# Performance work log

Measured on AMD Instinct MI355X. Metric: run time of the kernel, lower is better.

Reference implementation:

```python
import jax, jax.numpy as jnp
import numpy as np

N = 100000  # nodes
E = 1600000  # edges
D_IN, D_HID, D_OUT = 128, 128, 64
NEG_SLOPE = 0.2


def gat_conv(x, src, dst, W_src, W_dst, att_src, att_dst, bias, num_nodes):
    # PyG GATConv, heads=1, add_self_loops=False.
    h_src = x @ W_src          # [N, C]
    h_dst = x @ W_dst          # [N, C]
    a_src = (h_src * att_src).sum(-1)   # [N]
    a_dst = (h_dst * att_dst).sum(-1)   # [N]
    logits = jax.nn.leaky_relu(a_src[src] + a_dst[dst], NEG_SLOPE)  # [E]
    # segment softmax over destination neighborhoods
    seg_max = jax.ops.segment_max(logits, dst, num_segments=num_nodes)  # [N]
    e = jnp.exp(logits - seg_max[dst])
    denom = jax.ops.segment_sum(e, dst, num_segments=num_nodes)         # [N]
    alpha = e / (denom[dst] + 1e-16)                                    # [E]
    out = jax.ops.segment_sum(alpha[:, None] * h_src[src], dst, num_segments=num_nodes)  # [N, C]
    return out + bias


def setup_inputs() -> dict:
    key = jax.random.key(0)
    ks = jax.random.split(key, 12)
    x = jax.random.normal(ks[0], (N, D_IN), dtype=jnp.float32)
    edge_index = jax.random.randint(ks[1], (2, E), 0, N, dtype=jnp.int64)
    s1 = 1.0 / np.sqrt(D_IN)
    s2 = 1.0 / np.sqrt(D_HID)
    return {
        "x": x,
        "edge_index": edge_index,
        "W1_src": jax.random.uniform(ks[2], (D_IN, D_HID), jnp.float32, -s1, s1),
        "W1_dst": jax.random.uniform(ks[3], (D_IN, D_HID), jnp.float32, -s1, s1),
        "att1_src": jax.random.uniform(ks[4], (D_HID,), jnp.float32, -s2, s2),
        "att1_dst": jax.random.uniform(ks[5], (D_HID,), jnp.float32, -s2, s2),
        "b1": jnp.zeros((D_HID,), jnp.float32),
        "W2_src": jax.random.uniform(ks[6], (D_HID, D_OUT), jnp.float32, -s2, s2),
        "W2_dst": jax.random.uniform(ks[7], (D_HID, D_OUT), jnp.float32, -s2, s2),
        "att2_src": jax.random.uniform(ks[8], (D_OUT,), jnp.float32, -1.0 / np.sqrt(D_OUT), 1.0 / np.sqrt(D_OUT)),
        "att2_dst": jax.random.uniform(ks[9], (D_OUT,), jnp.float32, -1.0 / np.sqrt(D_OUT), 1.0 / np.sqrt(D_OUT)),
        "b2": jnp.zeros((D_OUT,), jnp.float32),
    }


def reference(x, edge_index, W1_src, W1_dst, att1_src, att1_dst, b1,
              W2_src, W2_dst, att2_src, att2_dst, b2):
    src, dst = edge_index[0], edge_index[1]
    h = gat_conv(x, src, dst, W1_src, W1_dst, att1_src, att1_dst, b1, N)
    h = jax.nn.relu(h)
    out = gat_conv(h, src, dst, W2_src, W2_dst, att2_src, att2_dst, b2, N)
    return out
```

## Files before the change

### kernel.cpp

```cpp
#include <hip/hip_runtime.h>


typedef unsigned long long u64;
typedef float v4f __attribute__((ext_vector_type(4)));
typedef _Float16 v2h __attribute__((ext_vector_type(2)));
typedef __fp16 h8 __attribute__((ext_vector_type(8)));

#define SEL_LO 0x01000504u
#define SEL_HI 0x03020706u

__device__ __forceinline__ void ntstore4(float* p, v4f v) {
    __builtin_nontemporal_store(v, (v4f*)p);
}
__device__ __forceinline__ unsigned h2pack(float a, float b) {
    v2h h;
    h.x = (_Float16)a;
    h.y = (_Float16)b;
    return __builtin_bit_cast(unsigned, h);
}
__device__ __forceinline__ float fdot2u(unsigned u, v2h w, float acc) {
    return __builtin_amdgcn_fdot2(__builtin_bit_cast(v2h, u), w, acc, false);
}
__device__ __forceinline__ v2h pkrtz(float a, float b) {
    return __builtin_bit_cast(v2h, __builtin_amdgcn_cvt_pkrtz(a, b));
}

__device__ void matvec_body(const float* __restrict__ W, const float* __restrict__ a,
                            float* __restrict__ out, int cols, int row) {
    int lane = threadIdx.x & 63;
    float s = 0.f;
    for (int j = lane; j < cols; j += 64) s += W[row * cols + j] * a[j];
#pragma unroll
    for (int o = 32; o; o >>= 1) s += __shfl_xor(s, o, 64);
    if (lane == 0) out[row] = s;
}

template <int C>
__device__ void packw_body(const float* __restrict__ W, uint4* __restrict__ Wp) {
    constexpr int NT = C / 16;
    const int total = 4 * NT * 64;
    for (int e = threadIdx.x; e < total; e += 256) {
        int lane = e & 63;
        int ti = (e >> 6) % NT;
        int t = (e >> 6) / NT;
        int k0 = 32 * t + (lane >> 4) * 8;
        int n = ti * 16 + (lane & 15);
        unsigned u[4];
#pragma unroll
        for (int p = 0; p < 4; ++p)
            u[p] = h2pack(W[(size_t)(k0 + 2 * p) * C + n], W[(size_t)(k0 + 2 * p + 1) * C + n]);
        Wp[e] = make_uint4(u[0], u[1], u[2], u[3]);
    }
}

__global__ __launch_bounds__(256) void setup_kernel(
    const int* __restrict__ dst, int* __restrict__ hist, int E, int nbE,
    const float* __restrict__ W1s, uint4* __restrict__ wp1,
    const float* __restrict__ W2s, uint4* __restrict__ wp2,
    const float* __restrict__ W1d, const float* __restrict__ att1d, float* __restrict__ watt1,
    const float* __restrict__ W2d, const float* __restrict__ att2d, float* __restrict__ watt2) {
    int b = blockIdx.x;
    if (b < nbE) {
        __shared__ int h[256];
        h[threadIdx.x] = 0;
        __syncthreads();
        int base = b * 4096;
        int lim = min(base + 4096, E);
        for (int i = base + threadIdx.x; i < lim; i += 256)
            atomicAdd(&h[__builtin_nontemporal_load(dst + i) >> 9], 1);
        __syncthreads();
        __builtin_nontemporal_store(h[threadIdx.x], hist + b * 256 + threadIdx.x);
    } else if (b == nbE) {
        packw_body<128>(W1s, wp1);
    } else if (b == nbE + 1) {
        packw_body<64>(W2s, wp2);
    } else if (b < nbE + 34) {
        matvec_body(W1d, att1d, watt1, 128, (b - nbE - 2) * 4 + (threadIdx.x >> 6));
    } else {
        matvec_body(W2d, att2d, watt2, 64, (b - nbE - 34) * 4 + (threadIdx.x >> 6));
    }
}

__global__ __launch_bounds__(256) void bscan_kernel(const int* __restrict__ hist, int nbE,
                                                    int* __restrict__ bbase,
                                                    int* __restrict__ gcur,
                                                    int* __restrict__ offs, int N, int E) {
    __shared__ int s[256];
    int t = threadIdx.x;
    int v = 0;
#pragma unroll 4
    for (int b = 0; b < nbE; ++b) v += hist[b * 256 + t];
    s[t] = v;
    __syncthreads();
    for (int o = 1; o < 256; o <<= 1) {
        int u = (t >= o) ? s[t - o] : 0;
        __syncthreads();
        s[t] += u;
        __syncthreads();
    }
    int excl = s[t] - v;
    bbase[t] = excl;
    gcur[t] = excl;
    if (t == 255) { bbase[256] = E; offs[N] = E; }
}

__device__ void scatter_body(const int* __restrict__ src, const int* __restrict__ dst,
                             int* __restrict__ gcur, u64* __restrict__ pairs, int E,
                             int blk, char* smem) {
    int* h = (int*)smem;
    int* sbase = h + 256;
    int* rbase = h + 512;
    u64* buf = (u64*)(smem + 3072);
    const int tid = threadIdx.x;
    h[tid] = 0;
    __syncthreads();
    const int base = blk * 4096;
    const int lim = min(4096, E - base);
    u64 pv[16];
    int rk[16];
    int bk[16];
#pragma unroll 16
    for (int k = 0; k < 16; ++k) {
        int i = base + k * 256 + tid;
        if (i < E) {
            int d = __builtin_nontemporal_load(dst + i);
            int b = d >> 9;
            bk[k] = b;
            pv[k] = ((u64)(unsigned)d << 32) | (unsigned)__builtin_nontemporal_load(src + i);
            rk[k] = atomicAdd(&h[b], 1);
        } else {
            bk[k] = -1;
        }
    }
    __syncthreads();
    const int v = h[tid];
    sbase[tid] = v;
    __syncthreads();
    for (int o = 1; o < 256; o <<= 1) {
        int uu = (tid >= o) ? sbase[tid - o] : 0;
        __syncthreads();
        sbase[tid] += uu;
        __syncthreads();
    }
    const int excl = sbase[tid] - v;
    rbase[tid] = v ? atomicAdd(&gcur[tid], v) : 0;
    __syncthreads();
    sbase[tid] = excl;
    __syncthreads();
#pragma unroll 16
    for (int k = 0; k < 16; ++k)
        if (bk[k] >= 0) buf[sbase[bk[k]] + rk[k]] = pv[k];
    __syncthreads();
    for (int i = tid; i < lim; i += 256) {
        u64 p = buf[i];
        int b = (int)(p >> 41);
        __builtin_nontemporal_store(p, pairs + (size_t)rbase[b] + (i - sbase[b]));
    }
}

__global__ __launch_bounds__(512) void bsort_kernel(const u64* __restrict__ pairs,
                                                    const int* __restrict__ bbase,
                                                    int* __restrict__ offs,
                                                    int* __restrict__ srcs, int N) {
    __shared__ int h[512];
    __shared__ int cur[512];
    const int t = threadIdx.x;
    const int b = blockIdx.x;
    const int beg = bbase[b], end = bbase[b + 1];
    h[t] = 0;
    __syncthreads();
    for (int i = beg + t; i < end; i += 512)
        atomicAdd(&h[(int)(__builtin_nontemporal_load(pairs + i) >> 32) & 511], 1);
    __syncthreads();
    int v = h[t];
    cur[t] = v;
    __syncthreads();
    for (int o = 1; o < 512; o <<= 1) {
        int u = (t >= o) ? cur[t - o] : 0;
        __syncthreads();
        cur[t] += u;
        __syncthreads();
    }
    int pos0 = beg + cur[t] - v;
    __syncthreads();
    cur[t] = pos0;
    int g = (b << 9) + t;
    if (g < N) offs[g] = pos0;
    __syncthreads();
    for (int i = beg + t; i < end; i += 512) {
        u64 p = __builtin_nontemporal_load(pairs + i);
        int local = (int)(p >> 32) & 511;
        int pp = atomicAdd(&cur[local], 1);
        srcs[pp] = (int)(p & 0xffffffffu);
    }
}

template <int C, bool XF16>
__device__ void gemm_body(int blk, const void* __restrict__ Xv, const uint4* __restrict__ Wp,
                          const float* __restrict__ attS, const float* __restrict__ wda,
                          unsigned* __restrict__ H, float* __restrict__ aS,
                          float* __restrict__ aD, int M, _Float16* hsAll) {
    constexpr int NT = C / 16;
    const int tid = threadIdx.x;
    const int w = tid >> 6;
    const int lane = tid & 63;
    const int l15 = lane & 15;
    const int q = lane >> 4;
    const int mb = blk * 64 + w * 16;
    const int m = mb + l15;
    const bool mv = m < M;

    v4f acc[NT];
#pragma unroll
    for (int n = 0; n < NT; ++n) acc[n] = (v4f)(0.f);
    float pd = 0.f;
    uint4 afu[4];

    if constexpr (XF16) {
        const uint4* Xp = (const uint4*)Xv + (size_t)m * 16;
#pragma unroll
        for (int t = 0; t < 4; ++t) {
            uint4 u = make_uint4(0u, 0u, 0u, 0u);
            if (mv) u = Xp[4 * t + q];
            afu[t] = u;
            const float* wdp = wda + 32 * t + 8 * q;
            pd = fdot2u(u.x, pkrtz(wdp[0], wdp[1]), pd);
            pd = fdot2u(u.y, pkrtz(wdp[2], wdp[3]), pd);
            pd = fdot2u(u.z, pkrtz(wdp[4], wdp[5]), pd);
            pd = fdot2u(u.w, pkrtz(wdp[6], wdp[7]), pd);
        }
    } else {
        const float* Xp = (const float*)Xv + (size_t)m * 128;
#pragma unroll
        for (int t = 0; t < 4; ++t) {
            float4 x0 = make_float4(0.f, 0.f, 0.f, 0.f);
            float4 x1 = x0;
            if (mv) {
                x0 = *(const float4*)(Xp + 32 * t + 8 * q);
                x1 = *(const float4*)(Xp + 32 * t + 8 * q + 4);
            }
            const float* wdp = wda + 32 * t + 8 * q;
            pd += x0.x * wdp[0] + x0.y * wdp[1] + x0.z * wdp[2] + x0.w * wdp[3] +
                  x1.x * wdp[4] + x1.y * wdp[5] + x1.z * wdp[6] + x1.w * wdp[7];
            afu[t] = make_uint4(h2pack(x0.x, x0.y), h2pack(x0.z, x0.w),
                                h2pack(x1.x, x1.y), h2pack(x1.z, x1.w));
        }
    }

#pragma unroll
    for (int t = 0; t < 4; ++t) {
        h8 a = __builtin_bit_cast(h8, afu[t]);
        const uint4* wp = Wp + (size_t)t * NT * 64 + lane;
#pragma unroll
        for (int n = 0; n < NT; ++n) {
            h8 b = __builtin_bit_cast(h8, wp[n * 64]);
            acc[n] = __builtin_amdgcn_mfma_f32_16x16x32_f16(a, b, acc[n], 0, 0, 0);
        }
    }

    pd += __shfl_xor(pd, 16, 64);
    pd += __shfl_xor(pd, 32, 64);
    if (q == 0 && mv) aD[m] = pd;

    float as4[4] = {0.f, 0.f, 0.f, 0.f};
#pragma unroll
    for (int n = 0; n < NT; ++n) {
        float av = attS[n * 16 + l15];
#pragma unroll
        for (int r = 0; r < 4; ++r) as4[r] += acc[n][r] * av;
    }
#pragma unroll
    for (int r = 0; r < 4; ++r) {
#pragma unroll
        for (int o = 1; o < 16; o <<= 1) as4[r] += __shfl_xor(as4[r], o, 64);
    }
    if (l15 == 0) {
#pragma unroll
        for (int r = 0; r < 4; ++r) {
            int row = mb + q * 4 + r;
            if (row < M) aS[row] = as4[r];
        }
    }

    _Float16* hp = hsAll + w * (16 * 136);
#pragma unroll
    for (int n = 0; n < NT; ++n)
#pragma unroll
        for (int r = 0; r < 4; ++r)
            hp[(q * 4 + r) * 136 + n * 16 + l15] = (_Float16)acc[n][r];

    constexpr int CH = C / 32;
    if (lane < 16 * CH) {
        int row = lane / CH;
        int ch = lane % CH;
        const uint4* rp = (const uint4*)(hp + row * 136 + ch * 32);
        uint4 v0 = rp[0], v1 = rp[1], v2 = rp[2], v3 = rp[3];
        int gr = mb + row;
        if (gr < M) {
            uint4* op = (uint4*)(H + (size_t)gr * (C / 2)) + ch * 4;
            op[0] = v0; op[1] = v1; op[2] = v2; op[3] = v3;
        }
    }
}

template <int C, bool XF16>
__global__ __launch_bounds__(256) void gemm_att_kernel(
    const void* __restrict__ Xv, const uint4* __restrict__ Wp,
    const float* __restrict__ attS, const float* __restrict__ wda,
    unsigned* __restrict__ H, float* __restrict__ aS, float* __restrict__ aD, int M) {
    __shared__ _Float16 hs[4 * 16 * 136];
    gemm_body<C, XF16>(blockIdx.x, Xv, Wp, attS, wda, H, aS, aD, M, hs);
}

__global__ __launch_bounds__(256) void scatter_gemm_kernel(
    const int* __restrict__ src, const int* __restrict__ dst, int* __restrict__ gcur,
    u64* __restrict__ pairs, int E, int nbS,
    const void* __restrict__ Xv, const uint4* __restrict__ Wp,
    const float* __restrict__ attS, const float* __restrict__ wda,
    unsigned* __restrict__ H, float* __restrict__ aS, float* __restrict__ aD, int M) {
    __shared__ __align__(16) char smem[35840];
    int b = blockIdx.x;
    if (b < nbS) scatter_body(src, dst, gcur, pairs, E, b, smem);
    else gemm_body<128, false>(b - nbS, Xv, Wp, attS, wda, H, aS, aD, M, (_Float16*)smem);
}

template <int C, bool RELU, bool F16OUT, bool NTOUT>
__global__ __launch_bounds__(256) void aggregate_kernel(
    const int* __restrict__ offs, const int* __restrict__ srcs,
    const unsigned* __restrict__ hsrc, const float* __restrict__ attS,
    const float* __restrict__ aS, const float* __restrict__ aD,
    const float* __restrict__ bias, void* __restrict__ outv, int n) {
    const int lane = threadIdx.x & 63;
    const int sl = lane & 31;
    const int hb = lane & 32;
    const int g = (lane >> 4) & 1;
    const int l = lane & 15;
    int node = (int)((blockIdx.x * blockDim.x + threadIdx.x) >> 5);
    if (node >= n) return;

    const int beg = offs[node], end = offs[node + 1];
    const int deg = end - beg;
    const float ad = aD[node];

    constexpr int LW = C / 32;
    constexpr int NA = C / 16;
    float acc[NA];
#pragma unroll
    for (int i = 0; i < NA; ++i) acc[i] = 0.f;

    v2h ash[LW];
    {
        const float* ap = attS + l * (2 * LW);
#pragma unroll
        for (int k = 0; k < LW; ++k)
            ash[k] = __builtin_bit_cast(v2h, h2pack(ap[2 * k], ap[2 * k + 1]));
    }

    int sj = 0;
    float u = 0.f;

    auto ldrow = [&](int s, unsigned* r) {
        if constexpr (C == 128) {
            uint4 v = ((const uint4*)(hsrc + ((size_t)s << 6)))[l];
            r[0] = v.x; r[1] = v.y; r[2] = v.z; r[3] = v.w;
        } else {
            uint2 v = ((const uint2*)(hsrc + ((size_t)s << 5)))[l];
            r[0] = v.x; r[1] = v.y;
        }
    };
    auto issue = [&](int j, unsigned (*buf)[LW]) {
        int e0 = hb + j * 8 + g;
        int s0 = __shfl(sj, e0, 64);
        int s1 = __shfl(sj, e0 + 2, 64);
        int s2 = __shfl(sj, e0 + 4, 64);
        int s3 = __shfl(sj, e0 + 6, 64);
        ldrow(s0, buf[0]);
        ldrow(s1, buf[1]);
        ldrow(s2, buf[2]);
        ldrow(s3, buf[3]);
    };

    auto edot = [&](int j, unsigned (*buf)[LW]) -> float {
        float d0 = 0.f, d1 = 0.f, d2 = 0.f, d3 = 0.f;
#pragma unroll
        for (int k = 0; k < LW; ++k) {
            d0 = fdot2u(buf[0][k], ash[k], d0);
            d1 = fdot2u(buf[1][k], ash[k], d1);
            d2 = fdot2u(buf[2][k], ash[k], d2);
            d3 = fdot2u(buf[3][k], ash[k], d3);
        }
        bool h8 = (l & 8) != 0;
        float a = (h8 ? d1 : d0) + __shfl_xor(h8 ? d0 : d1, 8, 64);
        float b = (h8 ? d3 : d2) + __shfl_xor(h8 ? d2 : d3, 8, 64);
        bool h4 = (l & 4) != 0;
        float c = (h4 ? b : a) + __shfl_xor(h4 ? a : b, 4, 64);
        c += __shfl_xor(c, 2, 64);
        c += __shfl_xor(c, 1, 64);
        int bsel = ((l >> 3) & 1) | (((l >> 2) & 1) << 1);
        int slot = j * 8 + g + 2 * bsel;
        float lg = c + ad;
        lg = (lg > 0.f) ? lg : 0.2f * lg;
        float uu = __expf(lg);
        return (slot < deg) ? uu : 0.f;
    };

    auto dotacc = [&](unsigned (*buf)[LW], v2h w01, v2h w23) {
#pragma unroll
        for (int ii = 0; ii < LW; ++ii) {
            acc[2 * ii] = fdot2u(__builtin_amdgcn_perm(buf[0][ii], buf[1][ii], SEL_LO), w01,
                          fdot2u(__builtin_amdgcn_perm(buf[2][ii], buf[3][ii], SEL_LO), w23, acc[2 * ii]));
            acc[2 * ii + 1] = fdot2u(__builtin_amdgcn_perm(buf[0][ii], buf[1][ii], SEL_HI), w01,
                              fdot2u(__builtin_amdgcn_perm(buf[2][ii], buf[3][ii], SEL_HI), w23, acc[2 * ii + 1]));
        }
    };

    auto computeF = [&](unsigned (*buf)[LW], float uj, float inv) {
        int bse = lane & 48;
        float w0 = __shfl(uj, bse + 0, 64) * inv;
        float w1 = __shfl(uj, bse + 8, 64) * inv;
        float w2 = __shfl(uj, bse + 4, 64) * inv;
        float w3 = __shfl(uj, bse + 12, 64) * inv;
        dotacc(buf, pkrtz(w0, w1), pkrtz(w2, w3));
    };

    auto computeS = [&](int j, unsigned (*buf)[LW], float inv) {
        int e0 = hb + j * 8 + g;
        float w0 = __shfl(u, e0, 64) * inv, w1 = __shfl(u, e0 + 2, 64) * inv;
        float w2 = __shfl(u, e0 + 4, 64) * inv, w3 = __shfl(u, e0 + 6, 64) * inv;
        dotacc(buf, pkrtz(w0, w1), pkrtz(w2, w3));
    };

    unsigned A0[4][LW], A1[4][LW], A2[4][LW], A3[4][LW];

    if (deg <= 32) {
        int i = beg + sl;
        if (i < end) sj = __builtin_nontemporal_load(srcs + i);
        int jm = (deg + 7) >> 3;
        if (jm > 0) issue(0, A0);
        if (jm > 1) issue(1, A1);
        if (jm > 2) issue(2, A2);
        if (jm > 3) issue(3, A3);
        float u0 = 0.f, u1 = 0.f, u2 = 0.f, u3 = 0.f;
        if (jm > 0) u0 = edot(0, A0);
        if (jm > 1) u1 = edot(1, A1);
        if (jm > 2) u2 = edot(2, A2);
        if (jm > 3) u3 = edot(3, A3);
        float t = (u0 + u1) + (u2 + u3);
        t += __shfl_xor(t, 8, 64);
        t += __shfl_xor(t, 4, 64);
        t += __shfl_xor(t, 16, 64);
        float inv = 1.f / (t + 1e-16f);
        if (jm > 0) computeF(A0, u0, inv);
        if (jm > 1) computeF(A1, u1, inv);
        if (jm > 2) computeF(A2, u2, inv);
        if (jm > 3) computeF(A3, u3, inv);
    } else {
        float m = -INFINITY;
        for (int i = beg + sl; i < end; i += 32) {
            float lg = aS[srcs[i]] + ad;
            lg = (lg > 0.f) ? lg : 0.2f * lg;
            m = fmaxf(m, lg);
        }
#pragma unroll
        for (int o = 16; o; o >>= 1) m = fmaxf(m, __shfl_xor(m, o, 64));
        float ssum = 0.f;
        for (int i = beg + sl; i < end; i += 32) {
            float lg = aS[srcs[i]] + ad;
            lg = (lg > 0.f) ? lg : 0.2f * lg;
            ssum += __expf(lg - m);
        }
#pragma unroll
        for (int o = 16; o; o >>= 1) ssum += __shfl_xor(ssum, o, 64);
        float inv = 1.f / (ssum + 1e-16f);
        for (int base = beg; base < end; base += 32) {
            int i = base + sl;
            sj = 0;
            u = 0.f;
            if (i < end) {
                sj = srcs[i];
                float lg = aS[sj] + ad;
                lg = (lg > 0.f) ? lg : 0.2f * lg;
                u = __expf(lg - m);
            }
            int cnt = min(32, end - base);
            int cj = (cnt + 7) >> 3;
            if (cj > 0) issue(0, A0);
            if (cj > 1) issue(1, A1);
            if (cj > 2) issue(2, A2);
            if (cj > 3) issue(3, A3);
            if (cj > 0) computeS(0, A0, inv);
            if (cj > 1) computeS(1, A1, inv);
            if (cj > 2) computeS(2, A2, inv);
            if (cj > 3) computeS(3, A3, inv);
        }
    }

#pragma unroll
    for (int i = 0; i < NA; ++i) acc[i] += __shfl_xor(acc[i], 16, 64);

    if (sl < 16) {
        float o[NA];
        const float* bp = bias + l * NA;
#pragma unroll
        for (int i = 0; i < NA; ++i) {
            o[i] = acc[i] + bp[i];
            if (RELU) o[i] = fmaxf(o[i], 0.f);
        }
        if constexpr (F16OUT) {
            unsigned uo[NA / 2];
#pragma unroll
            for (int k = 0; k < NA / 2; ++k) uo[k] = h2pack(o[2 * k], o[2 * k + 1]);
            unsigned* op = (unsigned*)outv + (size_t)node * (C / 2) + l * (NA / 2);
            if constexpr (NA == 8) *(uint4*)op = make_uint4(uo[0], uo[1], uo[2], uo[3]);
            else *(uint2*)op = make_uint2(uo[0], uo[1]);
        } else {
            float* op = (float*)outv + (size_t)node * C + l * NA;
#pragma unroll
            for (int q = 0; q < NA / 4; ++q) {
                v4f ov;
                ov.x = o[q * 4 + 0]; ov.y = o[q * 4 + 1];
                ov.z = o[q * 4 + 2]; ov.w = o[q * 4 + 3];
                if (NTOUT) ntstore4(op + q * 4, ov);
                else *(v4f*)(op + q * 4) = ov;
            }
        }
    }
}

extern "C" void kernel_launch(void* const* d_in, const int* in_sizes, int n_in,
                              void* d_out, int out_size, void* d_ws, size_t ws_size,
                              hipStream_t stream) {
    const float* x     = (const float*)d_in[0];
    const int*   edge  = (const int*)d_in[1];
    const float* W1s   = (const float*)d_in[2];
    const float* W1d   = (const float*)d_in[3];
    const float* att1s = (const float*)d_in[4];
    const float* att1d = (const float*)d_in[5];
    const float* b1    = (const float*)d_in[6];
    const float* W2s   = (const float*)d_in[7];
    const float* W2d   = (const float*)d_in[8];
    const float* att2s = (const float*)d_in[9];
    const float* att2d = (const float*)d_in[10];
    const float* b2    = (const float*)d_in[11];

    const int N = in_sizes[0] / 128;
    const int E = in_sizes[1] / 2;
    const int* srcI = edge;
    const int* dstI = edge + E;

    const int nbE = (E + 4095) / 4096;
    const int nbuckets = (N + 511) >> 9;
    const int gblk = (N + 63) / 64;

    size_t off = 0;
    auto alloc = [&](size_t bytes) {
        void* p = (char*)d_ws + off;
        off += (bytes + 255) & ~(size_t)255;
        return p;
    };
    int*      offs  = (int*)alloc((size_t)(N + 1) * 4);
    int*      srcs  = (int*)alloc((size_t)E * 4);
    int*      hist  = (int*)alloc((size_t)nbE * 256 * 4);
    int*      bbase = (int*)alloc(257 * 4);
    int*      gcur  = (int*)alloc(256 * 4);
    float*    watt1 = (float*)alloc(128 * 4);
    float*    watt2 = (float*)alloc(128 * 4);
    uint4*    wp1   = (uint4*)alloc(4 * 8 * 64 * 16);
    uint4*    wp2   = (uint4*)alloc(4 * 4 * 64 * 16);
    float*    a_s   = (float*)alloc((size_t)N * 4);
    float*    a_d   = (float*)alloc((size_t)N * 4);
    unsigned* g1h   = (unsigned*)alloc((size_t)N * 128 * 2);
    unsigned* h1h   = (unsigned*)alloc((size_t)N * 128 * 2);
    unsigned* g2h   = (unsigned*)alloc((size_t)N * 64 * 2);
    u64*      pairs = (u64*)h1h;

    setup_kernel<<<nbE + 66, 256, 0, stream>>>(dstI, hist, E, nbE, W1s, wp1, W2s, wp2,
                                               W1d, att1d, watt1, W2d, att2d, watt2);
    bscan_kernel<<<1, 256, 0, stream>>>(hist, nbE, bbase, gcur, offs, N, E);
    scatter_gemm_kernel<<<nbE + gblk, 256, 0, stream>>>(srcI, dstI, gcur, pairs, E, nbE,
                                                        x, wp1, att1s, watt1, g1h, a_s, a_d, N);
    bsort_kernel<<<nbuckets, 512, 0, stream>>>(pairs, bbase, offs, srcs, N);
    aggregate_kernel<128, true, true, false><<<(N + 7) / 8, 256, 0, stream>>>(
        offs, srcs, g1h, att1s, a_s, a_d, b1, h1h, N);
    gemm_att_kernel<64, true><<<gblk, 256, 0, stream>>>(h1h, wp2, att2s, watt2, g2h, a_s, a_d, N);
    aggregate_kernel<64, false, false, true><<<(N + 7) / 8, 256, 0, stream>>>(
        offs, srcs, g2h, att2s, a_s, a_d, b2, d_out, N);
}
```

Measured before the change: 329.1 us.

## Read precomputed source scores in aggregation and double-buffer row loads

The low-degree path of the aggregation kernel no longer recomputes each source's attention score with an fp16 dot product over the gathered feature row. It gathers the precomputed per-node aS value instead, which drops the edot shuffle reduction and the attS register preload. Row buffers shrink from four to two, and loads for the third and fourth edge groups are issued after the first two groups are consumed. This aims to free registers for occupancy, at the cost of less memory-level parallelism per wave and an extra scattered aS gather per edge.

```diff
diff --git a/kernel.cpp b/kernel.cpp
--- a/kernel.cpp
+++ b/kernel.cpp
@@ -327,9 +327,9 @@
 template <int C, bool RELU, bool F16OUT, bool NTOUT>
 __global__ __launch_bounds__(256) void aggregate_kernel(
     const int* __restrict__ offs, const int* __restrict__ srcs,
-    const unsigned* __restrict__ hsrc, const float* __restrict__ attS,
-    const float* __restrict__ aS, const float* __restrict__ aD,
-    const float* __restrict__ bias, void* __restrict__ outv, int n) {
+    const unsigned* __restrict__ hsrc, const float* __restrict__ aS,
+    const float* __restrict__ aD, const float* __restrict__ bias,
+    void* __restrict__ outv, int n) {
     const int lane = threadIdx.x & 63;
     const int sl = lane & 31;
     const int hb = lane & 32;
@@ -347,14 +347,6 @@
     float acc[NA];
 #pragma unroll
     for (int i = 0; i < NA; ++i) acc[i] = 0.f;
-
-    v2h ash[LW];
-    {
-        const float* ap = attS + l * (2 * LW);
-#pragma unroll
-        for (int k = 0; k < LW; ++k)
-            ash[k] = __builtin_bit_cast(v2h, h2pack(ap[2 * k], ap[2 * k + 1]));
-    }
 
     int sj = 0;
     float u = 0.f;
@@ -379,32 +371,12 @@
         ldrow(s2, buf[2]);
         ldrow(s3, buf[3]);
     };
-
-    auto edot = [&](int j, unsigned (*buf)[LW]) -> float {
-        float d0 = 0.f, d1 = 0.f, d2 = 0.f, d3 = 0.f;
-#pragma unroll
-        for (int k = 0; k < LW; ++k) {
-            d0 = fdot2u(buf[0][k], ash[k], d0);
-            d1 = fdot2u(buf[1][k], ash[k], d1);
-            d2 = fdot2u(buf[2][k], ash[k], d2);
-            d3 = fdot2u(buf[3][k], ash[k], d3);
-        }
-        bool h8 = (l & 8) != 0;
-        float a = (h8 ? d1 : d0) + __shfl_xor(h8 ? d0 : d1, 8, 64);
-        float b = (h8 ? d3 : d2) + __shfl_xor(h8 ? d2 : d3, 8, 64);
-        bool h4 = (l & 4) != 0;
-        float c = (h4 ? b : a) + __shfl_xor(h4 ? a : b, 4, 64);
-        c += __shfl_xor(c, 2, 64);
-        c += __shfl_xor(c, 1, 64);
-        int bsel = ((l >> 3) & 1) | (((l >> 2) & 1) << 1);
-        int slot = j * 8 + g + 2 * bsel;
-        float lg = c + ad;
-        lg = (lg > 0.f) ? lg : 0.2f * lg;
-        float uu = __expf(lg);
-        return (slot < deg) ? uu : 0.f;
-    };
-
-    auto dotacc = [&](unsigned (*buf)[LW], v2h w01, v2h w23) {
+    auto compute = [&](int j, unsigned (*buf)[LW], float inv) {
+        int e0 = hb + j * 8 + g;
+        float w0 = __shfl(u, e0, 64) * inv, w1 = __shfl(u, e0 + 2, 64) * inv;
+        float w2 = __shfl(u, e0 + 4, 64) * inv, w3 = __shfl(u, e0 + 6, 64) * inv;
+        v2h w01 = pkrtz(w0, w1);
+        v2h w23 = pkrtz(w2, w3);
 #pragma unroll
         for (int ii = 0; ii < LW; ++ii) {
             acc[2 * ii] = fdot2u(__builtin_amdgcn_perm(buf[0][ii], buf[1][ii], SEL_LO), w01,
@@ -414,46 +386,27 @@
         }
     };
 
-    auto computeF = [&](unsigned (*buf)[LW], float uj, float inv) {
-        int bse = lane & 48;
-        float w0 = __shfl(uj, bse + 0, 64) * inv;
-        float w1 = __shfl(uj, bse + 8, 64) * inv;
-        float w2 = __shfl(uj, bse + 4, 64) * inv;
-        float w3 = __shfl(uj, bse + 12, 64) * inv;
-        dotacc(buf, pkrtz(w0, w1), pkrtz(w2, w3));
-    };
-
-    auto computeS = [&](int j, unsigned (*buf)[LW], float inv) {
-        int e0 = hb + j * 8 + g;
-        float w0 = __shfl(u, e0, 64) * inv, w1 = __shfl(u, e0 + 2, 64) * inv;
-        float w2 = __shfl(u, e0 + 4, 64) * inv, w3 = __shfl(u, e0 + 6, 64) * inv;
-        dotacc(buf, pkrtz(w0, w1), pkrtz(w2, w3));
-    };
-
-    unsigned A0[4][LW], A1[4][LW], A2[4][LW], A3[4][LW];
+    unsigned A0[4][LW], A1[4][LW];
 
     if (deg <= 32) {
         int i = beg + sl;
-        if (i < end) sj = __builtin_nontemporal_load(srcs + i);
+        if (i < end) {
+            sj = __builtin_nontemporal_load(srcs + i);
+            float lg = aS[sj] + ad;
+            lg = (lg > 0.f) ? lg : 0.2f * lg;
+            u = __expf(lg);
+        }
         int jm = (deg + 7) >> 3;
         if (jm > 0) issue(0, A0);
         if (jm > 1) issue(1, A1);
-        if (jm > 2) issue(2, A2);
-        if (jm > 3) issue(3, A3);
-        float u0 = 0.f, u1 = 0.f, u2 = 0.f, u3 = 0.f;
-        if (jm > 0) u0 = edot(0, A0);
-        if (jm > 1) u1 = edot(1, A1);
-        if (jm > 2) u2 = edot(2, A2);
-        if (jm > 3) u3 = edot(3, A3);
-        float t = (u0 + u1) + (u2 + u3);
-        t += __shfl_xor(t, 8, 64);
-        t += __shfl_xor(t, 4, 64);
-        t += __shfl_xor(t, 16, 64);
-        float inv = 1.f / (t + 1e-16f);
-        if (jm > 0) computeF(A0, u0, inv);
-        if (jm > 1) computeF(A1, u1, inv);
-        if (jm > 2) computeF(A2, u2, inv);
-        if (jm > 3) computeF(A3, u3, inv);
+        float s = u;
+#pragma unroll
+        for (int o = 16; o; o >>= 1) s += __shfl_xor(s, o, 64);
+        float inv = 1.f / (s + 1e-16f);
+        if (jm > 0) { compute(0, A0, inv); if (jm > 2) issue(2, A0); }
+        if (jm > 1) { compute(1, A1, inv); if (jm > 3) issue(3, A1); }
+        if (jm > 2) compute(2, A0, inv);
+        if (jm > 3) compute(3, A1, inv);
     } else {
         float m = -INFINITY;
         for (int i = beg + sl; i < end; i += 32) {
@@ -486,12 +439,10 @@
             int cj = (cnt + 7) >> 3;
             if (cj > 0) issue(0, A0);
             if (cj > 1) issue(1, A1);
-            if (cj > 2) issue(2, A2);
-            if (cj > 3) issue(3, A3);
-            if (cj > 0) computeS(0, A0, inv);
-            if (cj > 1) computeS(1, A1, inv);
-            if (cj > 2) computeS(2, A2, inv);
-            if (cj > 3) computeS(3, A3, inv);
+            if (cj > 0) { compute(0, A0, inv); if (cj > 2) issue(2, A0); }
+            if (cj > 1) { compute(1, A1, inv); if (cj > 3) issue(3, A1); }
+            if (cj > 2) compute(2, A0, inv);
+            if (cj > 3) compute(3, A1, inv);
         }
     }
 
@@ -581,8 +532,8 @@
                                                         x, wp1, att1s, watt1, g1h, a_s, a_d, N);
     bsort_kernel<<<nbuckets, 512, 0, stream>>>(pairs, bbase, offs, srcs, N);
     aggregate_kernel<128, true, true, false><<<(N + 7) / 8, 256, 0, stream>>>(
-        offs, srcs, g1h, att1s, a_s, a_d, b1, h1h, N);
+        offs, srcs, g1h, a_s, a_d, b1, h1h, N);
     gemm_att_kernel<64, true><<<gblk, 256, 0, stream>>>(h1h, wp2, att2s, watt2, g2h, a_s, a_d, N);
     aggregate_kernel<64, false, false, true><<<(N + 7) / 8, 256, 0, stream>>>(
-        offs, srcs, g2h, att2s, a_s, a_d, b2, d_out, N);
-}
+        offs, srcs, g2h, a_s, a_d, b2, d_out, N);
+}
```

After: 316.6 us. 1.04x faster.
